# Performance work log

Hardware: AMD Instinct MI355X
Metric: run time of the kernel (lower is better)

The kernel has to match this reference:

```python
import jax, jax.numpy as jnp
import numpy as np

B, S, C = 8, 2048, 1024
DROPOUT_RATE = 0.1


def setup_inputs() -> dict:
    key = jax.random.key(0)
    k1, k2, k3 = jax.random.split(key, 3)
    x = jax.random.normal(k1, (B, S, C), dtype=jnp.float32)
    # Fixed orthogonal projection buffer, as in __init__: U from SVD of a random matrix
    rand_mat = jax.random.normal(k2, (C, C), dtype=jnp.float32)
    U, _, _ = jnp.linalg.svd(rand_mat)
    U = U.astype(jnp.float32)
    # Base random permutation of [0, C)
    perm = jax.random.permutation(k3, C).astype(jnp.int32)
    # Stand-in for random.randint(0, 1000), fixed for determinism
    randint = 123
    return {"x": x, "U": U, "perm": perm, "randint": randint}


def reference(x, U, perm, randint):
    # channel_dim == -1, so the transpose in the original forward is a no-op.
    rand_scale = (DROPOUT_RATE / (1.0 - DROPOUT_RATE)) ** 0.5
    n = x.shape[-1]
    b = x.size // n
    # _randperm_like: per-row permutation ans[b_, i] = perm[i] * (6*randint*b_ + 1) mod n.
    # Reduce the multiplier mod n first so int32 arithmetic never overflows
    # (math is identical since (a*b) % n == (a*(b%n)) % n).
    batch_rand = (jnp.arange(b, dtype=jnp.int32) * (randint * 6) + 1) % n  # [b]
    ans = (perm[None, :] * batch_rand[:, None]) % n                        # [b, n]
    ans = ans.reshape(x.shape)                                             # same shape as x

    x_g = jnp.take_along_axis(x, ans, axis=-1)   # gather per-row permuted channels
    y = jnp.matmul(x_g, U)                        # shared (C,C) projection
    # scatter_(-1, ans, y) places y[..., j] at position ans[..., j]; since ans is a
    # permutation per row, this equals gathering y with the inverse permutation.
    inv = jnp.argsort(ans, axis=-1)
    x_next = jnp.take_along_axis(y, inv, axis=-1)
    return x_next * rand_scale + x
```

## Files before the change

kernel.cpp:

```cpp
#include <hip/hip_runtime.h>
#include <hip/hip_bf16.h>

#define WS_UT    ((size_t)0)
#define WS_XG    ((size_t)2*1024*1024)

typedef __attribute__((ext_vector_type(8))) short short8;
typedef __attribute__((ext_vector_type(4))) float floatx4;

__device__ __forceinline__ void load_lds16(const void* g, void* l) {
  __builtin_amdgcn_global_load_lds(
      (const __attribute__((address_space(1))) void*)g,
      (__attribute__((address_space(3))) void*)l, 16, 0, 0);
}

__device__ __forceinline__ unsigned short f2bf(float f) {
  __hip_bfloat16 h = __float2bfloat16(f);
  return __builtin_bit_cast(unsigned short, h);
}
__device__ __forceinline__ float bf2f(unsigned short u) {
  return __uint_as_float(((unsigned)u) << 16);
}

__global__ void __launch_bounds__(256) prep_gather_k(const float* __restrict__ U,
                                                     const float* __restrict__ x,
                                                     const int* __restrict__ perm,
                                                     const int* __restrict__ prand,
                                                     unsigned short* __restrict__ ut,
                                                     unsigned short* __restrict__ xg) {
  __shared__ __align__(16) char smem[64 * 65 * 4];
  if (blockIdx.x < 256) {
    float (*tile)[65] = (float (*)[65])smem;
    const int tn = (blockIdx.x & 15) * 64;
    const int tk = (blockIdx.x >> 4) * 64;
    const int r = threadIdx.x >> 6;
    const int c = threadIdx.x & 63;
    for (int s = 0; s < 16; ++s)
      tile[s * 4 + r][c] = U[(size_t)(tk + s * 4 + r) * 1024 + tn + c];
    __syncthreads();
    for (int s = 0; s < 16; ++s)
      ut[(size_t)(tn + s * 4 + r) * 1024 + tk + c] = f2bf(tile[c][s * 4 + r]);
    return;
  }
  float (*xrow)[1024] = (float (*)[1024])smem;
  const int w = threadIdx.x >> 6, lane = threadIdx.x & 63;
  const int row = (blockIdx.x - 256) * 4 + w;
  const unsigned mult = ((unsigned)prand[0] * 6u) & 1023u;
  const unsigned br = (((unsigned)row & 1023u) * mult + 1u) & 1023u;
  const float* xr = x + (size_t)row * 1024;
  unsigned short* xo = xg + (size_t)row * 1024;
  for (int t = 0; t < 4; ++t) {
    floatx4 v = *(const floatx4*)(xr + t * 256 + lane * 4);
    *(floatx4*)(&xrow[w][t * 256 + lane * 4]) = v;
  }
  __syncthreads();
  for (int t = 0; t < 4; ++t) {
    int i0 = t * 256 + lane * 4;
    int4 p = *(const int4*)(perm + i0);
    ushort4 o;
    o.x = f2bf(xrow[w][((unsigned)p.x * br) & 1023u]);
    o.y = f2bf(xrow[w][((unsigned)p.y * br) & 1023u]);
    o.z = f2bf(xrow[w][((unsigned)p.z * br) & 1023u]);
    o.w = f2bf(xrow[w][((unsigned)p.w * br) & 1023u]);
    *(ushort4*)(xo + i0) = o;
  }
}

__global__ void __launch_bounds__(512, 1) gemm_scatter_k(
    const unsigned short* __restrict__ xg,
    const unsigned short* __restrict__ ut,
    const int* __restrict__ perm,
    const int* __restrict__ prand,
    float* __restrict__ out) {
  extern __shared__ __align__(16) char smem[];
  char* Abuf = smem;
  char* Bbuf = smem + 8192;
  const int tid = threadIdx.x;
  const int w = tid >> 6, lane = tid & 63;
  const int m = lane & 15, q = lane >> 4;
  const int R0 = blockIdx.x * 64;
  const int wn = w * 128;

  const int x3 = m & 7;
  const int qq = q ^ (x3 & 3);
  const int sf = x3 >> 2;
  const int offF0 = m * 128 + (qq + sf * 4) * 16;
  const int offF1 = m * 128 + (qq + 4 - sf * 4) * 16;

  const int sr = lane >> 3, sslot = lane & 7;
  const unsigned short* asrc =
      xg + (size_t)(R0 + w * 8 + sr) * 1024 + (size_t)((sslot ^ sr) * 8);
  char* adst = Abuf + w * 1024 + lane * 16;
  const unsigned short* bsrc =
      ut + (size_t)(w * 128 + sr) * 1024 + (size_t)((sslot ^ sr) * 8);
  char* bdst = Bbuf + w * 16384 + lane * 16;

  floatx4 acc[4][8];
#pragma unroll
  for (int i = 0; i < 4; ++i)
#pragma unroll
    for (int jj = 0; jj < 8; ++jj) acc[i][jj] = (floatx4)0.0f;

#pragma unroll 1
  for (int kt = 0; kt < 16; ++kt) {
    const int k0 = kt * 64;
    load_lds16(asrc + k0, adst);
#pragma unroll
    for (int t = 0; t < 16; ++t)
      load_lds16(bsrc + (size_t)t * 8192 + k0, bdst + t * 1024);
    __syncthreads();
    short8 a0[4], b0[8];
#pragma unroll
    for (int i = 0; i < 4; ++i) a0[i] = *(const short8*)(Abuf + i * 2048 + offF0);
#pragma unroll
    for (int jj = 0; jj < 8; ++jj)
      b0[jj] = *(const short8*)(Bbuf + wn * 128 + jj * 2048 + offF0);
#pragma unroll
    for (int i = 0; i < 4; ++i)
#pragma unroll
      for (int jj = 0; jj < 8; ++jj)
        acc[i][jj] = __builtin_amdgcn_mfma_f32_16x16x32_bf16(b0[jj], a0[i],
                                                             acc[i][jj], 0, 0, 0);
    short8 a1[4], b1[8];
#pragma unroll
    for (int i = 0; i < 4; ++i) a1[i] = *(const short8*)(Abuf + i * 2048 + offF1);
#pragma unroll
    for (int jj = 0; jj < 8; ++jj)
      b1[jj] = *(const short8*)(Bbuf + wn * 128 + jj * 2048 + offF1);
#pragma unroll
    for (int i = 0; i < 4; ++i)
#pragma unroll
      for (int jj = 0; jj < 8; ++jj)
        acc[i][jj] = __builtin_amdgcn_mfma_f32_16x16x32_bf16(b1[jj], a1[i],
                                                             acc[i][jj], 0, 0, 0);
    __syncthreads();
  }

  const unsigned mult = ((unsigned)prand[0] * 6u) & 1023u;
  const float rs = 0.33333334f;
  float* sbuf = (float*)smem;
#pragma unroll
  for (int i = 0; i < 4; ++i) {
    const int row = R0 + i * 16 + m;
    const unsigned br = (((unsigned)row & 1023u) * mult + 1u) & 1023u;
    const unsigned short* xr = xg + (size_t)row * 1024;
#pragma unroll
    for (int jj = 0; jj < 8; ++jj) {
      const int j0 = wn + jj * 16 + q * 4;
      const int4 p4 = *(const int4*)(perm + j0);
      const ushort4 x4 = *(const ushort4*)(xr + j0);
      sbuf[m * 1024 + (((unsigned)p4.x * br) & 1023u)] = rs * acc[i][jj][0] + bf2f(x4.x);
      sbuf[m * 1024 + (((unsigned)p4.y * br) & 1023u)] = rs * acc[i][jj][1] + bf2f(x4.y);
      sbuf[m * 1024 + (((unsigned)p4.z * br) & 1023u)] = rs * acc[i][jj][2] + bf2f(x4.z);
      sbuf[m * 1024 + (((unsigned)p4.w * br) & 1023u)] = rs * acc[i][jj][3] + bf2f(x4.w);
    }
    __syncthreads();
    float* orow0 = out + (size_t)(R0 + i * 16) * 1024;
#pragma unroll
    for (int v = 0; v < 8; ++v) {
      const int f = v * 512 + tid;
      *(floatx4*)(orow0 + ((f >> 8) * 1024 + (f & 255) * 4)) =
          *(const floatx4*)(sbuf + (size_t)f * 4);
    }
    if (i < 3) __syncthreads();
  }
}

extern "C" void kernel_launch(void* const* d_in, const int* in_sizes, int n_in,
                              void* d_out, int out_size, void* d_ws, size_t ws_size,
                              hipStream_t stream) {
  const float* x = (const float*)d_in[0];
  const float* U = (const float*)d_in[1];
  const int* perm = (const int*)d_in[2];
  const int* prand = (const int*)d_in[3];
  float* out = (float*)d_out;
  char* ws = (char*)d_ws;
  unsigned short* ut = (unsigned short*)(ws + WS_UT);
  unsigned short* xg = (unsigned short*)(ws + WS_XG);

  hipFuncSetAttribute((const void*)gemm_scatter_k,
                      hipFuncAttributeMaxDynamicSharedMemorySize, 139264);

  prep_gather_k<<<256 + 4096, 256, 0, stream>>>(U, x, perm, prand, ut, xg);
  gemm_scatter_k<<<256, 512, 139264, stream>>>(xg, ut, perm, prand, out);
}
```

Baseline: 172.0 us.

## Double-buffer GEMM K-loop with async LDS prefetch and finer K steps

Restructures the GEMM main loop from 16 synchronous K=64 steps into 32 K=32 steps with two LDS buffers. The next stage's global-to-LDS loads are issued before computing on the current one, using explicit vmcnt waits and raw barriers, so global memory latency can overlap MFMA work. The LDS layout and swizzle change to match the 32-wide K chunks. The trade is twice as many barriers, less MFMA work per barrier, and hand-tuned vmcnt counts that must match the per-wave load counts exactly.

```diff
diff --git a/kernel.cpp b/kernel.cpp
--- a/kernel.cpp
+++ b/kernel.cpp
@@ -72,27 +72,21 @@
     const int* __restrict__ prand,
     float* __restrict__ out) {
   extern __shared__ __align__(16) char smem[];
-  char* Abuf = smem;
-  char* Bbuf = smem + 8192;
   const int tid = threadIdx.x;
   const int w = tid >> 6, lane = tid & 63;
   const int m = lane & 15, q = lane >> 4;
   const int R0 = blockIdx.x * 64;
   const int wn = w * 128;
 
-  const int x3 = m & 7;
-  const int qq = q ^ (x3 & 3);
-  const int sf = x3 >> 2;
-  const int offF0 = m * 128 + (qq + sf * 4) * 16;
-  const int offF1 = m * 128 + (qq + 4 - sf * 4) * 16;
+  const int cR = (q ^ ((m >> 1) & 3)) * 16;
+  const int offA = m * 64 + cR;
+  const int offB = w * 8192 + m * 64 + cR;
 
-  const int sr = lane >> 3, sslot = lane & 7;
-  const unsigned short* asrc =
-      xg + (size_t)(R0 + w * 8 + sr) * 1024 + (size_t)((sslot ^ sr) * 8);
-  char* adst = Abuf + w * 1024 + lane * 16;
-  const unsigned short* bsrc =
-      ut + (size_t)(w * 128 + sr) * 1024 + (size_t)((sslot ^ sr) * 8);
-  char* bdst = Bbuf + w * 16384 + lane * 16;
+  const int srow = lane >> 2;
+  const int schunk = ((lane & 3) ^ ((lane >> 3) & 3)) * 8;
+  const unsigned short* bsrc = ut + (size_t)(w * 128 + srow) * 1024 + schunk;
+  const unsigned short* asrc = xg + (size_t)(R0 + w * 16 + srow) * 1024 + schunk;
+  const int ldst = lane * 16;
 
   floatx4 acc[4][8];
 #pragma unroll
@@ -100,40 +94,47 @@
 #pragma unroll
     for (int jj = 0; jj < 8; ++jj) acc[i][jj] = (floatx4)0.0f;
 
-#pragma unroll 1
-  for (int kt = 0; kt < 16; ++kt) {
-    const int k0 = kt * 64;
-    load_lds16(asrc + k0, adst);
+  auto stage = [&](int h) {
+    const int k0 = h * 32;
+    char* Ab = smem + (h & 1) * 4096;
+    char* Bb = smem + 8192 + (h & 1) * 65536;
 #pragma unroll
-    for (int t = 0; t < 16; ++t)
-      load_lds16(bsrc + (size_t)t * 8192 + k0, bdst + t * 1024);
-    __syncthreads();
-    short8 a0[4], b0[8];
+    for (int t = 0; t < 8; ++t)
+      load_lds16(bsrc + (size_t)t * 16384 + k0, Bb + w * 8192 + t * 1024 + ldst);
+    if (w < 4) load_lds16(asrc + k0, Ab + w * 1024 + ldst);
+  };
+
+  stage(0);
 #pragma unroll
-    for (int i = 0; i < 4; ++i) a0[i] = *(const short8*)(Abuf + i * 2048 + offF0);
+  for (int h = 0; h < 32; ++h) {
+    if (h < 31) {
+      stage(h + 1);
+      if (w < 4) asm volatile("s_waitcnt vmcnt(9)" ::: "memory");
+      else       asm volatile("s_waitcnt vmcnt(8)" ::: "memory");
+    } else {
+      asm volatile("s_waitcnt vmcnt(0)" ::: "memory");
+    }
+    __builtin_amdgcn_sched_barrier(0);
+    __builtin_amdgcn_s_barrier();
+    __builtin_amdgcn_sched_barrier(0);
+    const char* Ab = smem + (h & 1) * 4096;
+    const char* Bb = smem + 8192 + (h & 1) * 65536;
+    short8 a[4], b[8];
 #pragma unroll
-    for (int jj = 0; jj < 8; ++jj)
-      b0[jj] = *(const short8*)(Bbuf + wn * 128 + jj * 2048 + offF0);
+    for (int i = 0; i < 4; ++i) a[i] = *(const short8*)(Ab + i * 1024 + offA);
+#pragma unroll
+    for (int jj = 0; jj < 8; ++jj) b[jj] = *(const short8*)(Bb + jj * 1024 + offB);
 #pragma unroll
     for (int i = 0; i < 4; ++i)
 #pragma unroll
       for (int jj = 0; jj < 8; ++jj)
-        acc[i][jj] = __builtin_amdgcn_mfma_f32_16x16x32_bf16(b0[jj], a0[i],
+        acc[i][jj] = __builtin_amdgcn_mfma_f32_16x16x32_bf16(b[jj], a[i],
                                                              acc[i][jj], 0, 0, 0);
-    short8 a1[4], b1[8];
-#pragma unroll
-    for (int i = 0; i < 4; ++i) a1[i] = *(const short8*)(Abuf + i * 2048 + offF1);
-#pragma unroll
-    for (int jj = 0; jj < 8; ++jj)
-      b1[jj] = *(const short8*)(Bbuf + wn * 128 + jj * 2048 + offF1);
-#pragma unroll
-    for (int i = 0; i < 4; ++i)
-#pragma unroll
-      for (int jj = 0; jj < 8; ++jj)
-        acc[i][jj] = __builtin_amdgcn_mfma_f32_16x16x32_bf16(b1[jj], a1[i],
-                                                             acc[i][jj], 0, 0, 0);
-    __syncthreads();
+    __builtin_amdgcn_sched_barrier(0);
+    __builtin_amdgcn_s_barrier();
+    __builtin_amdgcn_sched_barrier(0);
   }
+  __syncthreads();
 
   const unsigned mult = ((unsigned)prand[0] * 6u) & 1023u;
   const float rs = 0.33333334f;
```

Result: slower. 176.1 us (+2.4%).
